# Kernel optimization log

Measured on AMD Instinct MI355X. Metric: run time of the kernel, lower is better.

Reference implementation:

```python
import jax, jax.numpy as jnp
import numpy as np

B, IN, H = 4096, 1024, 1024


def setup_inputs() -> dict:
    key = jax.random.key(0)
    ks = jax.random.split(key, 12)
    s = float(np.sqrt(6.0 / (IN + H)))  # xavier-uniform-like scale
    u = lambda k, shp: jax.random.uniform(k, shp, jnp.float32, -s, s)
    return {
        "x": jax.random.normal(ks[0], (B, IN), jnp.float32),
        "h_prev": jax.random.normal(ks[1], (B, H), jnp.float32),
        "c_prev": jax.random.normal(ks[2], (B, H), jnp.float32),
        "n_prev": jnp.ones((B, H), jnp.float32),
        "m_prev": jnp.zeros((B, H), jnp.float32),
        "Wi_x": u(ks[3], (H, IN)), "bi": jnp.zeros((H,), jnp.float32), "Wi_h": u(ks[4], (H, H)),
        "Wf_x": u(ks[5], (H, IN)), "bf": jnp.full((H,), 2.0, jnp.float32), "Wf_h": u(ks[6], (H, H)),
        "Wz_x": u(ks[7], (H, IN)), "bz": jnp.zeros((H,), jnp.float32), "Wz_h": u(ks[8], (H, H)),
        "Wo_x": u(ks[9], (H, IN)), "bo": jnp.zeros((H,), jnp.float32), "Wo_h": u(ks[10], (H, H)),
    }


def reference(x, h_prev, c_prev, n_prev, m_prev,
              Wi_x, bi, Wi_h, Wf_x, bf, Wf_h,
              Wz_x, bz, Wz_h, Wo_x, bo, Wo_h):
    # 8 projections (x-side with bias, h-side without), torch Linear: y = x @ W.T + b
    i_tilde = x @ Wi_x.T + bi + h_prev @ Wi_h.T
    f_aff   = x @ Wf_x.T + bf + h_prev @ Wf_h.T
    z_aff   = x @ Wz_x.T + bz + h_prev @ Wz_h.T
    o_aff   = x @ Wo_x.T + bo + h_prev @ Wo_h.T

    # forget_as_exp=False path: sigmoid forget gate, log-domain stabilizer
    log_f = jnp.log(jnp.clip(jax.nn.sigmoid(f_aff), 1e-8, None))
    m_t = jnp.maximum(log_f + m_prev, i_tilde)
    i_prime = jnp.exp(i_tilde - m_t)
    f_prime = jnp.exp(log_f + m_prev - m_t)

    z = jnp.tanh(z_aff)
    c_t = f_prime * c_prev + i_prime * z
    n_t = f_prime * n_prev + i_prime
    h_t = jax.nn.sigmoid(o_aff) * (c_t / jnp.clip(n_t, 1e-6, None))
    return h_t, c_t, n_t, m_t
```

## Files before the change

### kernel.cpp

```cpp
#include <hip/hip_runtime.h>
#include <stdint.h>


#define B_DIM 4096
#define K_DIM 2048

typedef __bf16 bf16x8 __attribute__((ext_vector_type(8)));
typedef float f32x4 __attribute__((ext_vector_type(4)));
typedef unsigned short ushort8 __attribute__((ext_vector_type(8)));

__device__ __forceinline__ unsigned short f2bf(float f) {
  unsigned u = __float_as_uint(f);
  u += 0x7fffu + ((u >> 16) & 1u);
  return (unsigned short)(u >> 16);
}
__device__ __forceinline__ float bf2f(unsigned short u) {
  return __uint_as_float(((unsigned)u) << 16);
}

__device__ __forceinline__ ushort8 load8_as_bf16(const void* base, size_t off, bool isbf) {
  if (isbf) return *(const ushort8*)((const unsigned short*)base + off);
  const float* f = (const float*)base + off;
  float4 v0 = ((const float4*)f)[0];
  float4 v1 = ((const float4*)f)[1];
  ushort8 o;
  o[0] = f2bf(v0.x); o[1] = f2bf(v0.y); o[2] = f2bf(v0.z); o[3] = f2bf(v0.w);
  o[4] = f2bf(v1.x); o[5] = f2bf(v1.y); o[6] = f2bf(v1.z); o[7] = f2bf(v1.w);
  return o;
}

__global__ void pack_all(const void* __restrict__ xv, const void* __restrict__ hv,
                         const void* __restrict__ Wix, const void* __restrict__ Wih,
                         const void* __restrict__ Wfx, const void* __restrict__ Wfh,
                         const void* __restrict__ Wzx, const void* __restrict__ Wzh,
                         const void* __restrict__ Wox, const void* __restrict__ Woh,
                         unsigned short* __restrict__ Apk, unsigned short* __restrict__ Bpk) {
  const int blk = blockIdx.x;
  const int lane = threadIdx.x & 63;
  const bool isA = blk < 4096;
  const unsigned* disc = (const unsigned*)(isA ? xv : Wix);
  int v = 0;
  if (lane < 32) {
    unsigned e = (disc[lane] >> 7) & 0xFFu;
    v = (e > (isA ? 129u : 122u)) ? 1 : 0;
  }
  const bool isbf = (__ballot(v) == 0ull);

  const int k = threadIdx.x * 8;
  if (isA) {
    const int m = blk;
    const void* src = (k < 1024) ? xv : hv;
    size_t off = (size_t)m * 1024 + (k & 1023);
    *(ushort8*)(Apk + (size_t)m * 2048 + k) = load8_as_bf16(src, off, isbf);
  } else {
    const int br = blk - 4096;
    const int g = (br >> 4) & 3;
    const int wrow = ((br >> 6) << 4) | (br & 15);
    const void* W;
    if (k < 1024) W = (g == 0) ? Wix : (g == 1) ? Wfx : (g == 2) ? Wzx : Wox;
    else          W = (g == 0) ? Wih : (g == 1) ? Wfh : (g == 2) ? Wzh : Woh;
    size_t off = (size_t)wrow * 1024 + (k & 1023);
    *(ushort8*)(Bpk + (size_t)br * 2048 + k) = load8_as_bf16(W, off, isbf);
  }
}


__device__ __forceinline__ void gload16(const void* g, void* l) {
  __builtin_amdgcn_global_load_lds(
      (__attribute__((address_space(1))) void*)g,
      (__attribute__((address_space(3))) void*)l, 16, 0, 0);
}

#define SCHED0 __builtin_amdgcn_sched_barrier(0)
#define BAR    __builtin_amdgcn_s_barrier()
#define VM6    asm volatile("s_waitcnt vmcnt(6)" ::: "memory")
#define VM0    asm volatile("s_waitcnt vmcnt(0)" ::: "memory")
#define LGKM(N) asm volatile("s_waitcnt lgkmcnt(" #N ")" ::: "memory")
#define NOWAIT ((void)0)
#define NOSTAGE ((void)0)
#define MFMA16(a, b, c) __builtin_amdgcn_mfma_f32_16x16x32_bf16(a, b, c, 0, 0, 0)

#define STAGE_HALF(buf, ab, hf, kt) {                                          \
    _Pragma("unroll")                                                          \
    for (int r_ = 0; r_ < 2; ++r_) {                                           \
      const unsigned short* g_ = (ab ? sB : sA) +                              \
          (size_t)((r_ * 128 + (hf) * (ab ? 32 : 64)) * 2048 + (kt) * 64);     \
      gload16(g_, &lds[buf][ab][(hf) * 128 + r_ * 64 + w * 8][0]);             \
    } }

#define LDSA(buf, mh, mi, CS) \
  (*(const bf16x8*)(&lds[buf][0][0][0] + ((mh)*128 + (mi)*16)*64 + aBase + CS))
#define LDSB(buf, nh, nf, CS) \
  (*(const bf16x8*)(&lds[buf][1][0][0] + ((nh)*128 + (nf)*16)*64 + bBase + CS))

#define PH_Q00(buf, STG) {                                                     \
    LGKM(0); SCHED0; BAR; SCHED0;                                              \
    STG;                                                                       \
    fB1[0][0] = LDSB(buf, 1, 0, csw0); fB1[1][0] = LDSB(buf, 1, 1, csw0);      \
    fB1[0][1] = LDSB(buf, 1, 0, csw1); fB1[1][1] = LDSB(buf, 1, 1, csw1);      \
    __builtin_amdgcn_s_setprio(1);                                             \
    _Pragma("unroll") for (int mi = 0; mi < 4; ++mi)                           \
      _Pragma("unroll") for (int nf = 0; nf < 2; ++nf)                         \
        _Pragma("unroll") for (int ks = 0; ks < 2; ++ks)                       \
          acc[mi][nf] = MFMA16(fA[mi][ks], fB0[nf][ks], acc[mi][nf]);          \
    __builtin_amdgcn_s_setprio(0);                                             \
  }

#define PH_Q01(buf, STG) {                                                     \
    LGKM(0); SCHED0; BAR; SCHED0;                                              \
    STG;                                                                       \
    __builtin_amdgcn_s_setprio(1);                                             \
    _Pragma("unroll") for (int mi = 0; mi < 4; ++mi) {                         \
      _Pragma("unroll") for (int nf = 0; nf < 2; ++nf)                         \
        _Pragma("unroll") for (int ks = 0; ks < 2; ++ks)                       \
          acc[mi][2+nf] = MFMA16(fA[mi][ks], fB1[nf][ks], acc[mi][2+nf]);      \
      fA[mi][0] = LDSA(buf, 1, mi, csw0);                                      \
      fA[mi][1] = LDSA(buf, 1, mi, csw1);                                      \
    }                                                                          \
    __builtin_amdgcn_s_setprio(0);                                             \
  }

#define PH_Q11(STG) {                                                          \
    LGKM(0); SCHED0; BAR; SCHED0;                                              \
    STG;                                                                       \
    __builtin_amdgcn_s_setprio(1);                                             \
    _Pragma("unroll") for (int mi = 0; mi < 4; ++mi)                           \
      _Pragma("unroll") for (int nf = 0; nf < 2; ++nf)                         \
        _Pragma("unroll") for (int ks = 0; ks < 2; ++ks)                       \
          acc[4+mi][2+nf] = MFMA16(fA[mi][ks], fB1[nf][ks], acc[4+mi][2+nf]);  \
    __builtin_amdgcn_s_setprio(0);                                             \
  }

#define PH_Q10(nbuf, STG, VMW, RF) {                                           \
    VMW; SCHED0; BAR; SCHED0;                                                  \
    STG;                                                                       \
    __builtin_amdgcn_s_setprio(1);                                             \
    _Pragma("unroll") for (int mi = 0; mi < 4; ++mi)                           \
      _Pragma("unroll") for (int ks = 0; ks < 2; ++ks)                         \
        acc[4+mi][0] = MFMA16(fA[mi][ks], fB0[0][ks], acc[4+mi][0]);           \
    if (RF) { fB0[0][0] = LDSB(nbuf, 0, 0, csw0);                              \
              fB0[0][1] = LDSB(nbuf, 0, 0, csw1); }                            \
    _Pragma("unroll") for (int mi = 0; mi < 4; ++mi) {                         \
      _Pragma("unroll") for (int ks = 0; ks < 2; ++ks)                         \
        acc[4+mi][1] = MFMA16(fA[mi][ks], fB0[1][ks], acc[4+mi][1]);           \
      if (RF) { fA[mi][0] = LDSA(nbuf, 0, mi, csw0);                           \
                fA[mi][1] = LDSA(nbuf, 0, mi, csw1); }                         \
    }                                                                          \
    if (RF) { fB0[1][0] = LDSB(nbuf, 0, 1, csw0);                              \
              fB0[1][1] = LDSB(nbuf, 0, 1, csw1); }                            \
    __builtin_amdgcn_s_setprio(0);                                             \
  }

__global__ __launch_bounds__(512, 2) void gemm_fused(
    const unsigned short* __restrict__ Apk,
    const unsigned short* __restrict__ Bpk,
    const void* __restrict__ bi, const void* __restrict__ bfg,
    const void* __restrict__ bz, const void* __restrict__ bo,
    const void* __restrict__ c_prev, const void* __restrict__ n_prev,
    const void* __restrict__ m_prev,
    float* __restrict__ out)
{
  __shared__ unsigned short lds[2][2][256][64];

  const int tid  = threadIdx.x;
  const int w    = tid >> 6;
  const int lane = tid & 63;
  const int wm   = w >> 2;
  const int wn   = w & 3;
  const int lcol = lane & 15;
  const int qrow = lane >> 4;

  const int bid = blockIdx.x;
  const int swz = (bid & 7) * 32 + (bid >> 3);
  const int bm = swz >> 4;
  const int bn = swz & 15;

  const int l3 = lane >> 3;
  const int cg = (lane & 7) ^ l3;
  const unsigned short* sA = Apk + (size_t)(bm * 256 + w * 8 + l3) * 2048 + cg * 8;
  const unsigned short* sB = Bpk + (size_t)(bn * 256 + (w >> 2) * 64 + (w & 3) * 8 + l3) * 2048 + cg * 8;

  const int csw0 = (((lane >> 4)    ) ^ (lane & 7)) * 8;
  const int csw1 = ((4 + (lane >> 4)) ^ (lane & 7)) * 8;
  const int aBase = (wm * 64 + lcol) * 64;
  const int bBase = (wn * 32 + lcol) * 64;

  f32x4 acc[8][4] = {};
  bf16x8 fA[4][2], fB0[2][2], fB1[2][2];

  STAGE_HALF(0, 0, 0, 0); SCHED0;
  STAGE_HALF(0, 1, 0, 0); SCHED0;
  STAGE_HALF(0, 1, 1, 0); SCHED0;
  STAGE_HALF(0, 0, 1, 0); SCHED0;
  STAGE_HALF(1, 0, 0, 1); SCHED0;
  STAGE_HALF(1, 1, 0, 1); SCHED0;
  STAGE_HALF(1, 1, 1, 1); SCHED0;
  STAGE_HALF(1, 0, 1, 1); SCHED0;
  asm volatile("s_waitcnt vmcnt(8)" ::: "memory"); SCHED0; BAR; SCHED0;
#pragma unroll
  for (int mi = 0; mi < 4; ++mi) {
    fA[mi][0] = LDSA(0, 0, mi, csw0);
    fA[mi][1] = LDSA(0, 0, mi, csw1);
  }
  fB0[0][0] = LDSB(0, 0, 0, csw0); fB0[0][1] = LDSB(0, 0, 0, csw1);
  fB0[1][0] = LDSB(0, 0, 1, csw0); fB0[1][1] = LDSB(0, 0, 1, csw1);

  for (int i = 0; i < 15; ++i) {
    const int tE = 2 * i + 2, tO = 2 * i + 3;
    PH_Q00(0, STAGE_HALF(0, 0, 0, tE));
    PH_Q01(0, STAGE_HALF(0, 1, 1, tE));
    PH_Q11(   STAGE_HALF(0, 0, 1, tE));
    PH_Q10(1, STAGE_HALF(0, 1, 0, tE), VM6, 1);
    PH_Q00(1, STAGE_HALF(1, 0, 0, tO));
    PH_Q01(1, STAGE_HALF(1, 1, 1, tO));
    PH_Q11(   STAGE_HALF(1, 0, 1, tO));
    PH_Q10(0, STAGE_HALF(1, 1, 0, tO), VM6, 1);
  }
  PH_Q00(0, NOSTAGE);
  PH_Q01(0, NOSTAGE);
  PH_Q11(   NOSTAGE);
  PH_Q10(1, NOSTAGE, VM0, 1);
  PH_Q00(1, NOSTAGE);
  PH_Q01(1, NOSTAGE);
  PH_Q11(   NOSTAGE);
  PH_Q10(0, NOSTAGE, NOWAIT, 0);

  const bool sbf = (((const unsigned*)n_prev)[0] == 0x3F803F80u);
  const bool bbf = (((const unsigned*)bfg)[0]    == 0x40004000u);
  const int bcol = wn * 16 + lcol;
  const int n = bn * 64 + bcol;
  const float bi_n = bbf ? bf2f(((const unsigned short*)bi)[n])  : ((const float*)bi)[n];
  const float bf_n = bbf ? bf2f(((const unsigned short*)bfg)[n]) : ((const float*)bfg)[n];
  const float bz_n = bbf ? bf2f(((const unsigned short*)bz)[n])  : ((const float*)bz)[n];
  const float bo_n = bbf ? bf2f(((const unsigned short*)bo)[n])  : ((const float*)bo)[n];

#define GATE_MATH                                                              \
      float sf = 1.f / (1.f + __expf(-fa));                                    \
      sf = fmaxf(sf, 1e-8f);                                                   \
      float lf_ = __logf(sf);                                                  \
      float mt = fmaxf(lf_ + mp, it);                                          \
      float ip = __expf(it - mt);                                              \
      float fp = __expf(lf_ + mp - mt);                                        \
      float zc = fminf(fmaxf(za, -15.f), 15.f);                                \
      float e2 = __expf(2.f * zc);                                             \
      float z  = (e2 - 1.f) / (e2 + 1.f);                                      \
      float ct = fp * cp + ip * z;                                             \
      float nt = fp * npv + ip;                                                \
      float so = 1.f / (1.f + __expf(-oa));                                    \
      float ht = so * (ct / fmaxf(nt, 1e-6f));

  if (!sbf) {
    float* lf = (float*)&lds[0][0][0][0];
    const float* srcC = (const float*)c_prev;
    const float* srcN = (const float*)n_prev;
    const float* srcM = (const float*)m_prev;

#pragma unroll
    for (int hh = 0; hh < 2; ++hh) {
#pragma unroll
      for (int s = 0; s < 3; ++s) {
        const float* srcp = (s == 0) ? srcC : (s == 1) ? srcN : srcM;
#pragma unroll
        for (int jj = 0; jj < 4; ++jj) {
          const int j = w * 4 + jj;
          const int lr = j * 4 + qrow;
          const int grow = bm * 256 + (lr >> 6) * 128 + hh * 64 + (lr & 63);
          const float* g = srcp + (size_t)grow * 1024 + bn * 64 + lcol * 4;
          gload16(g, lf + s * 8192 + j * 256);
        }
      }
      SCHED0; VM0; SCHED0; BAR; SCHED0;

      float gc[16], gn[16], gm[16];
#pragma unroll
      for (int ml = 0; ml < 4; ++ml)
#pragma unroll
        for (int r = 0; r < 4; ++r) {
          const int off = (wm * 64 + ml * 16 + qrow * 4 + r) * 64 + bcol;
          gc[ml * 4 + r] = lf[off];
          gn[ml * 4 + r] = lf[8192 + off];
          gm[ml * 4 + r] = lf[16384 + off];
        }
      SCHED0; LGKM(0); SCHED0; BAR; SCHED0;

#pragma unroll
      for (int ml = 0; ml < 4; ++ml) {
        const int mi = hh * 4 + ml;
#pragma unroll
        for (int r = 0; r < 4; ++r) {
          const int e = ml * 4 + r;
          float it = acc[mi][0][r] + bi_n;
          float fa = acc[mi][1][r] + bf_n;
          float za = acc[mi][2][r] + bz_n;
          float oa = acc[mi][3][r] + bo_n;
          float cp = gc[e], npv = gn[e], mp = gm[e];
          GATE_MATH
          const int off = (wm * 64 + ml * 16 + qrow * 4 + r) * 64 + bcol;
          lf[off]         = ht;
          lf[8192  + off] = ct;
          lf[16384 + off] = nt;
          lf[24576 + off] = mt;
        }
      }
      SCHED0; LGKM(0); SCHED0; BAR; SCHED0;

#pragma unroll
      for (int k = 0; k < 16; ++k) {
        const int c = k * 512 + tid;
        const int s = c >> 11;
        const int cs = c & 2047;
        const int lr = cs >> 4, c4 = cs & 15;
        f32x4 v = *(const f32x4*)(lf + s * 8192 + lr * 64 + c4 * 4);
        const int grow = bm * 256 + (lr >> 6) * 128 + hh * 64 + (lr & 63);
        *(f32x4*)(out + (size_t)s * 4194304 + (size_t)grow * 1024 + bn * 64 + c4 * 4) = v;
      }
      SCHED0; LGKM(0); SCHED0; BAR; SCHED0;
    }
  } else {
    const int row0 = bm * 256 + wm * 128 + qrow * 4;
    float* out_h = out;
    float* out_c = out + 4194304;
    float* out_n = out + 2 * 4194304;
    float* out_m = out + 3 * 4194304;
#pragma unroll
    for (int mi = 0; mi < 8; ++mi) {
#pragma unroll
      for (int r = 0; r < 4; ++r) {
        const int row = row0 + mi * 16 + r;
        const size_t idx = (size_t)row * 1024 + n;
        float it = acc[mi][0][r] + bi_n;
        float fa = acc[mi][1][r] + bf_n;
        float za = acc[mi][2][r] + bz_n;
        float oa = acc[mi][3][r] + bo_n;
        float cp  = bf2f(((const unsigned short*)c_prev)[idx]);
        float npv = bf2f(((const unsigned short*)n_prev)[idx]);
        float mp  = bf2f(((const unsigned short*)m_prev)[idx]);
        GATE_MATH
        out_h[idx] = ht;
        out_c[idx] = ct;
        out_n[idx] = nt;
        out_m[idx] = mt;
      }
    }
  }
#undef GATE_MATH
}

extern "C" void kernel_launch(void* const* d_in, const int* in_sizes, int n_in,
                              void* d_out, int out_size, void* d_ws, size_t ws_size,
                              hipStream_t stream) {
  const void* x      = d_in[0];
  const void* h_prev = d_in[1];
  const void* c_prev = d_in[2];
  const void* n_prev = d_in[3];
  const void* m_prev = d_in[4];
  const void* Wi_x = d_in[5];
  const void* bi   = d_in[6];
  const void* Wi_h = d_in[7];
  const void* Wf_x = d_in[8];
  const void* bf   = d_in[9];
  const void* Wf_h = d_in[10];
  const void* Wz_x = d_in[11];
  const void* bz   = d_in[12];
  const void* Wz_h = d_in[13];
  const void* Wo_x = d_in[14];
  const void* bo   = d_in[15];
  const void* Wo_h = d_in[16];

  unsigned short* Apk = (unsigned short*)d_ws;
  unsigned short* Bpk = Apk + (size_t)B_DIM * K_DIM;

  pack_all<<<8192, 256, 0, stream>>>(x, h_prev, Wi_x, Wi_h, Wf_x, Wf_h,
                                     Wz_x, Wz_h, Wo_x, Wo_h, Apk, Bpk);
  gemm_fused<<<256, 512, 0, stream>>>(Apk, Bpk, bi, bf, bz, bo,
                                      c_prev, n_prev, m_prev,
                                      (float*)d_out);
}
```

Before: 253.9 us.

## Prefetch state tensors during GEMM tail and store epilogue directly to global

The pack kernel now processes four rows per block with a quarter of the blocks, which cuts block launch overhead. In the fused GEMM, fp32 c/n/m state for the first half of rows is loaded into registers before the final MFMA phases so its latency overlaps the last compute. The LDS-staged epilogue with its barriers is replaced by direct per-element global loads and stores. This removes the synchronisation and LDS round trips, but it trades coalesced 16-byte stores for scattered 4-byte column stores and raises register pressure from 48 extra live floats.

```diff
diff --git a/kernel.cpp b/kernel.cpp
--- a/kernel.cpp
+++ b/kernel.cpp
@@ -37,7 +37,7 @@
                          unsigned short* __restrict__ Apk, unsigned short* __restrict__ Bpk) {
   const int blk = blockIdx.x;
   const int lane = threadIdx.x & 63;
-  const bool isA = blk < 4096;
+  const bool isA = blk < 1024;
   const unsigned* disc = (const unsigned*)(isA ? xv : Wix);
   int v = 0;
   if (lane < 32) {
@@ -47,20 +47,24 @@
   const bool isbf = (__ballot(v) == 0ull);
 
   const int k = threadIdx.x * 8;
-  if (isA) {
-    const int m = blk;
-    const void* src = (k < 1024) ? xv : hv;
-    size_t off = (size_t)m * 1024 + (k & 1023);
-    *(ushort8*)(Apk + (size_t)m * 2048 + k) = load8_as_bf16(src, off, isbf);
-  } else {
-    const int br = blk - 4096;
-    const int g = (br >> 4) & 3;
-    const int wrow = ((br >> 6) << 4) | (br & 15);
-    const void* W;
-    if (k < 1024) W = (g == 0) ? Wix : (g == 1) ? Wfx : (g == 2) ? Wzx : Wox;
-    else          W = (g == 0) ? Wih : (g == 1) ? Wfh : (g == 2) ? Wzh : Woh;
-    size_t off = (size_t)wrow * 1024 + (k & 1023);
-    *(ushort8*)(Bpk + (size_t)br * 2048 + k) = load8_as_bf16(W, off, isbf);
+  const int r0 = (isA ? blk : blk - 1024) * 4;
+#pragma unroll
+  for (int rr = 0; rr < 4; ++rr) {
+    if (isA) {
+      const int m = r0 + rr;
+      const void* src = (k < 1024) ? xv : hv;
+      size_t off = (size_t)m * 1024 + (k & 1023);
+      *(ushort8*)(Apk + (size_t)m * 2048 + k) = load8_as_bf16(src, off, isbf);
+    } else {
+      const int br = r0 + rr;
+      const int g = (br >> 4) & 3;
+      const int wrow = ((br >> 6) << 4) | (br & 15);
+      const void* W;
+      if (k < 1024) W = (g == 0) ? Wix : (g == 1) ? Wfx : (g == 2) ? Wzx : Wox;
+      else          W = (g == 0) ? Wih : (g == 1) ? Wfh : (g == 2) ? Wzh : Woh;
+      size_t off = (size_t)wrow * 1024 + (k & 1023);
+      *(ushort8*)(Bpk + (size_t)br * 2048 + k) = load8_as_bf16(W, off, isbf);
+    }
   }
 }
 
@@ -216,6 +220,27 @@
     PH_Q11(   STAGE_HALF(1, 0, 1, tO));
     PH_Q10(0, STAGE_HALF(1, 1, 0, tO), VM6, 1);
   }
+
+  const bool sbf = (((const unsigned*)n_prev)[0] == 0x3F803F80u);
+  const int n = bn * 64 + wn * 16 + lcol;
+  const int row0 = bm * 256 + wm * 128 + qrow * 4;
+  float pc[16], pn[16], pm[16];
+  if (!sbf) {
+    const float* Cp = (const float*)c_prev;
+    const float* Np = (const float*)n_prev;
+    const float* Mp = (const float*)m_prev;
+#pragma unroll
+    for (int mi = 0; mi < 4; ++mi)
+#pragma unroll
+      for (int r = 0; r < 4; ++r) {
+        const size_t idx = (size_t)(row0 + mi * 16 + r) * 1024 + n;
+        pc[mi * 4 + r] = Cp[idx];
+        pn[mi * 4 + r] = Np[idx];
+        pm[mi * 4 + r] = Mp[idx];
+      }
+  }
+  SCHED0;
+
   PH_Q00(0, NOSTAGE);
   PH_Q01(0, NOSTAGE);
   PH_Q11(   NOSTAGE);
@@ -225,14 +250,16 @@
   PH_Q11(   NOSTAGE);
   PH_Q10(0, NOSTAGE, NOWAIT, 0);
 
-  const bool sbf = (((const unsigned*)n_prev)[0] == 0x3F803F80u);
-  const bool bbf = (((const unsigned*)bfg)[0]    == 0x40004000u);
-  const int bcol = wn * 16 + lcol;
-  const int n = bn * 64 + bcol;
+  const bool bbf = (((const unsigned*)bfg)[0] == 0x40004000u);
   const float bi_n = bbf ? bf2f(((const unsigned short*)bi)[n])  : ((const float*)bi)[n];
   const float bf_n = bbf ? bf2f(((const unsigned short*)bfg)[n]) : ((const float*)bfg)[n];
   const float bz_n = bbf ? bf2f(((const unsigned short*)bz)[n])  : ((const float*)bz)[n];
   const float bo_n = bbf ? bf2f(((const unsigned short*)bo)[n])  : ((const float*)bo)[n];
+
+  float* out_h = out;
+  float* out_c = out + 4194304;
+  float* out_n = out + 2 * 4194304;
+  float* out_m = out + 3 * 4194304;
 
 #define GATE_MATH                                                              \
       float sf = 1.f / (1.f + __expf(-fa));                                    \
@@ -250,84 +277,63 @@
       float ht = so * (ct / fmaxf(nt, 1e-6f));
 
   if (!sbf) {
-    float* lf = (float*)&lds[0][0][0][0];
-    const float* srcC = (const float*)c_prev;
-    const float* srcN = (const float*)n_prev;
-    const float* srcM = (const float*)m_prev;
-
-#pragma unroll
-    for (int hh = 0; hh < 2; ++hh) {
-#pragma unroll
-      for (int s = 0; s < 3; ++s) {
-        const float* srcp = (s == 0) ? srcC : (s == 1) ? srcN : srcM;
-#pragma unroll
-        for (int jj = 0; jj < 4; ++jj) {
-          const int j = w * 4 + jj;
-          const int lr = j * 4 + qrow;
-          const int grow = bm * 256 + (lr >> 6) * 128 + hh * 64 + (lr & 63);
-          const float* g = srcp + (size_t)grow * 1024 + bn * 64 + lcol * 4;
-          gload16(g, lf + s * 8192 + j * 256);
+    float qc[16], qn[16], qm[16];
+    {
+      const float* Cp = (const float*)c_prev;
+      const float* Np = (const float*)n_prev;
+      const float* Mp = (const float*)m_prev;
+#pragma unroll
+      for (int ml = 0; ml < 4; ++ml)
+#pragma unroll
+        for (int r = 0; r < 4; ++r) {
+          const size_t idx = (size_t)(row0 + (4 + ml) * 16 + r) * 1024 + n;
+          qc[ml * 4 + r] = Cp[idx];
+          qn[ml * 4 + r] = Np[idx];
+          qm[ml * 4 + r] = Mp[idx];
         }
+    }
+    SCHED0;
+#pragma unroll
+    for (int mi = 0; mi < 4; ++mi)
+#pragma unroll
+      for (int r = 0; r < 4; ++r) {
+        const int e = mi * 4 + r;
+        const size_t idx = (size_t)(row0 + mi * 16 + r) * 1024 + n;
+        float it = acc[mi][0][r] + bi_n;
+        float fa = acc[mi][1][r] + bf_n;
+        float za = acc[mi][2][r] + bz_n;
+        float oa = acc[mi][3][r] + bo_n;
+        float cp = pc[e], npv = pn[e], mp = pm[e];
+        GATE_MATH
+        out_h[idx] = ht;
+        out_c[idx] = ct;
+        out_n[idx] = nt;
+        out_m[idx] = mt;
       }
-      SCHED0; VM0; SCHED0; BAR; SCHED0;
-
-      float gc[16], gn[16], gm[16];
-#pragma unroll
-      for (int ml = 0; ml < 4; ++ml)
-#pragma unroll
-        for (int r = 0; r < 4; ++r) {
-          const int off = (wm * 64 + ml * 16 + qrow * 4 + r) * 64 + bcol;
-          gc[ml * 4 + r] = lf[off];
-          gn[ml * 4 + r] = lf[8192 + off];
-          gm[ml * 4 + r] = lf[16384 + off];
-        }
-      SCHED0; LGKM(0); SCHED0; BAR; SCHED0;
-
-#pragma unroll
-      for (int ml = 0; ml < 4; ++ml) {
-        const int mi = hh * 4 + ml;
-#pragma unroll
-        for (int r = 0; r < 4; ++r) {
-          const int e = ml * 4 + r;
-          float it = acc[mi][0][r] + bi_n;
-          float fa = acc[mi][1][r] + bf_n;
-          float za = acc[mi][2][r] + bz_n;
-          float oa = acc[mi][3][r] + bo_n;
-          float cp = gc[e], npv = gn[e], mp = gm[e];
-          GATE_MATH
-          const int off = (wm * 64 + ml * 16 + qrow * 4 + r) * 64 + bcol;
-          lf[off]         = ht;
-          lf[8192  + off] = ct;
-          lf[16384 + off] = nt;
-          lf[24576 + off] = mt;
-        }
+#pragma unroll
+    for (int ml = 0; ml < 4; ++ml)
+#pragma unroll
+      for (int r = 0; r < 4; ++r) {
+        const int e = ml * 4 + r;
+        const int mi = 4 + ml;
+        const size_t idx = (size_t)(row0 + mi * 16 + r) * 1024 + n;
+        float it = acc[mi][0][r] + bi_n;
+        float fa = acc[mi][1][r] + bf_n;
+        float za = acc[mi][2][r] + bz_n;
+        float oa = acc[mi][3][r] + bo_n;
+        float cp = qc[e], npv = qn[e], mp = qm[e];
+        GATE_MATH
+        out_h[idx] = ht;
+        out_c[idx] = ct;
+        out_n[idx] = nt;
+        out_m[idx] = mt;
       }
-      SCHED0; LGKM(0); SCHED0; BAR; SCHED0;
-
-#pragma unroll
-      for (int k = 0; k < 16; ++k) {
-        const int c = k * 512 + tid;
-        const int s = c >> 11;
-        const int cs = c & 2047;
-        const int lr = cs >> 4, c4 = cs & 15;
-        f32x4 v = *(const f32x4*)(lf + s * 8192 + lr * 64 + c4 * 4);
-        const int grow = bm * 256 + (lr >> 6) * 128 + hh * 64 + (lr & 63);
-        *(f32x4*)(out + (size_t)s * 4194304 + (size_t)grow * 1024 + bn * 64 + c4 * 4) = v;
-      }
-      SCHED0; LGKM(0); SCHED0; BAR; SCHED0;
-    }
   } else {
-    const int row0 = bm * 256 + wm * 128 + qrow * 4;
-    float* out_h = out;
-    float* out_c = out + 4194304;
-    float* out_n = out + 2 * 4194304;
-    float* out_m = out + 3 * 4194304;
-#pragma unroll
-    for (int mi = 0; mi < 8; ++mi) {
+#pragma unroll
+    for (int mi = 0; mi < 8; ++mi)
 #pragma unroll
       for (int r = 0; r < 4; ++r) {
-        const int row = row0 + mi * 16 + r;
-        const size_t idx = (size_t)row * 1024 + n;
+        const size_t idx = (size_t)(row0 + mi * 16 + r) * 1024 + n;
         float it = acc[mi][0][r] + bi_n;
         float fa = acc[mi][1][r] + bf_n;
         float za = acc[mi][2][r] + bz_n;
@@ -341,7 +347,6 @@
         out_n[idx] = nt;
         out_m[idx] = mt;
       }
-    }
   }
 #undef GATE_MATH
 }
@@ -370,7 +375,7 @@
   unsigned short* Apk = (unsigned short*)d_ws;
   unsigned short* Bpk = Apk + (size_t)B_DIM * K_DIM;
 
-  pack_all<<<8192, 256, 0, stream>>>(x, h_prev, Wi_x, Wi_h, Wf_x, Wf_h,
+  pack_all<<<2048, 256, 0, stream>>>(x, h_prev, Wi_x, Wi_h, Wf_x, Wf_h,
                                      Wz_x, Wz_h, Wo_x, Wo_h, Apk, Bpk);
   gemm_fused<<<256, 512, 0, stream>>>(Apk, Bpk, bi, bf, bz, bo,
                                       c_prev, n_prev, m_prev,
```

Result: slower. 277.1 us (+9.1%).
